# Kernel optimization log

Hardware: AMD Instinct MI355X
Metric: run time of the kernel (lower is better)

Reference implementation:

```python
import jax, jax.numpy as jnp
import numpy as np


def setup_inputs() -> dict:
    key = jax.random.key(0)
    k1, k2, k3 = jax.random.split(key, 3)
    B, C, H, W = 16, 256, 32, 32
    K, D = 8192, 256
    z = jax.random.normal(k1, (B, C, H, W), dtype=jnp.float32)
    # torch init: uniform(-1/K, 1/K); use small-scale values for realism
    embedding = jax.random.uniform(k2, (K, D), dtype=jnp.float32,
                                   minval=-1.0 / K, maxval=1.0 / K)
    proj_w = jax.random.normal(k3, (D, D), dtype=jnp.float32) * (1.0 / np.sqrt(D))
    return {"z": z, "embedding": embedding, "proj_w": proj_w}


def reference(z, embedding, proj_w):
    commitment_cost = 0.25
    B, C, H, W = z.shape
    # codebook = Linear(embedding) with no bias: emb @ W^T  -> [K, D]
    codebook = embedding @ proj_w.T
    zt = jnp.transpose(z, (0, 2, 3, 1))            # [B, H, W, C]
    zf = zt.reshape(-1, C)                          # [N, C], N = B*H*W
    # squared distances: ||z||^2 + ||e||^2 - 2 z.e  -> [N, K]
    d = (jnp.sum(zf * zf, axis=1, keepdims=True)
         + jnp.sum(codebook * codebook, axis=1)
         - 2.0 * jnp.einsum('nd,kd->nk', zf, codebook))
    min_encoding_indices = jnp.argmin(d, axis=1)    # [N]
    z_quantized = codebook[min_encoding_indices].reshape(zt.shape)  # [B,H,W,C]
    commitment_loss = commitment_cost * jnp.mean(
        (jax.lax.stop_gradient(z_quantized) - zt) ** 2)
    codebook_loss = jnp.mean((z_quantized - jax.lax.stop_gradient(zt)) ** 2)
    loss = commitment_loss + codebook_loss
    # straight-through estimator
    zq_st = zt + jax.lax.stop_gradient(z_quantized - zt)
    out = jnp.transpose(zq_st, (0, 3, 1, 2))        # [B, C, H, W]
    idx = min_encoding_indices.reshape(B, H, W)
    return out, loss, commitment_loss, codebook_loss, idx
```

## Files before the change

kernel.cpp:

```cpp
#include <hip/hip_runtime.h>
#include <cfloat>


constexpr int Dd = 256;
constexpr float INV_M = 1.0f / 4194304.0f;
constexpr float DLT = 1e-3f;

typedef unsigned short u16;
typedef unsigned int u32;
typedef __attribute__((ext_vector_type(8))) short short8;
typedef __attribute__((ext_vector_type(4))) float f32x4;

#define GLOBAL_AS __attribute__((address_space(1)))
#define LDS_AS    __attribute__((address_space(3)))

__device__ __forceinline__ unsigned monof(float f) {
  unsigned u = __float_as_uint(f);
  return (u & 0x80000000u) ? ~u : (u | 0x80000000u);
}
__device__ __forceinline__ float unmonof(unsigned p) {
  unsigned u = (p & 0x80000000u) ? (p & 0x7FFFFFFFu) : ~p;
  return __uint_as_float(u);
}
__device__ __forceinline__ u16 f2bf(float x) {
  unsigned u = __float_as_uint(x);
  u += 0x7FFFu + ((u >> 16) & 1u);
  return (u16)(u >> 16);
}

__global__ __launch_bounds__(256)
void k_codebook(const float* __restrict__ emb, const float* __restrict__ proj,
                float* __restrict__ cb, u16* __restrict__ eh) {
  __shared__ float et[64 * 65];
  __shared__ float pt[64 * 65];
  const int t = threadIdx.x;
  const int tx = t & 15, ty = t >> 4;
  const int kb = blockIdx.x * 64;
  const int db = blockIdx.y * 64;
  float acc[4][4];
#pragma unroll
  for (int u = 0; u < 4; ++u)
#pragma unroll
    for (int v = 0; v < 4; ++v) acc[u][v] = 0.f;

  const int jm = t & 15;
  const int q  = t >> 4;

  for (int jc = 0; jc < Dd; jc += 64) {
    __syncthreads();
#pragma unroll
    for (int i = 0; i < 4; ++i) {
      const int row = q + i * 16;
      const float4 e4 = *(const float4*)(emb  + (size_t)(kb + row) * Dd + jc + jm * 4);
      const float4 p4 = *(const float4*)(proj + (size_t)(db + row) * Dd + jc + jm * 4);
      et[(jm*4 + 0) * 65 + row] = e4.x;
      et[(jm*4 + 1) * 65 + row] = e4.y;
      et[(jm*4 + 2) * 65 + row] = e4.z;
      et[(jm*4 + 3) * 65 + row] = e4.w;
      pt[(jm*4 + 0) * 65 + row] = p4.x;
      pt[(jm*4 + 1) * 65 + row] = p4.y;
      pt[(jm*4 + 2) * 65 + row] = p4.z;
      pt[(jm*4 + 3) * 65 + row] = p4.w;
    }
    __syncthreads();
#pragma unroll 16
    for (int j = 0; j < 64; ++j) {
      float a[4], b[4];
#pragma unroll
      for (int u = 0; u < 4; ++u) a[u] = et[j*65 + ty*4 + u];
#pragma unroll
      for (int v = 0; v < 4; ++v) b[v] = pt[j*65 + tx*4 + v];
#pragma unroll
      for (int u = 0; u < 4; ++u)
#pragma unroll
        for (int v = 0; v < 4; ++v) acc[u][v] = fmaf(a[u], b[v], acc[u][v]);
    }
  }
#pragma unroll
  for (int u = 0; u < 4; ++u) {
    const int k = kb + ty*4 + u;
#pragma unroll
    for (int v = 0; v < 4; ++v) {
      const int d = db + tx*4 + v;
      const float val = acc[u][v];
      cb[(size_t)k * Dd + d] = val;
      eh[(size_t)k * Dd + d] = f2bf(val);
    }
  }
}

__global__ __launch_bounds__(256)
void k_norms(const float* __restrict__ cb, float* __restrict__ norms) {
  const int k = blockIdx.x * 256 + threadIdx.x;
  const float* row = cb + (size_t)k * Dd;
  float s = 0.f;
  for (int d = 0; d < Dd; d += 4) {
    const float4 v = *(const float4*)(row + d);
    s = fmaf(v.x, v.x, s);
    s = fmaf(v.y, v.y, s);
    s = fmaf(v.z, v.z, s);
    s = fmaf(v.w, v.w, s);
  }
  norms[k] = s;
}

__global__ __launch_bounds__(256)
void k_prep_z(const float* __restrict__ z, u16* __restrict__ zh,
              float* __restrict__ znorm) {
  __shared__ float tile[256 * 33];
  const int t = threadIdx.x;
  const int blk = blockIdx.x;
  const int w = t & 31, rg = t >> 5;
  const size_t zbase = (size_t)(blk >> 5) * 262144 + (size_t)(blk & 31) * 32 + w;
#pragma unroll 8
  for (int i = 0; i < 32; ++i) {
    const int d = rg * 32 + i;
    tile[d * 33 + w] = z[zbase + (size_t)d * 1024];
  }
  __syncthreads();
  if (t < 32) {
    float s = 0.f;
    for (int d = 0; d < Dd; ++d) {
      const float v = tile[d * 33 + t];
      s = fmaf(v, v, s);
    }
    znorm[blk * 32 + t] = s;
  }
  const int nl = t >> 3, seg = t & 7;
  const size_t obase = (size_t)(blk * 32 + nl) * Dd + seg * 32;
#pragma unroll
  for (int j = 0; j < 4; ++j) {
    u16 hb[8];
#pragma unroll
    for (int e = 0; e < 8; ++e)
      hb[e] = f2bf(tile[(seg * 32 + j * 8 + e) * 33 + nl]);
    *(uint4*)(zh + obase + j * 8) = *(const uint4*)hb;
  }
}

template <bool EMIT>
__global__ __launch_bounds__(256, 2)
void k_scan(const u16* __restrict__ zh, const u16* __restrict__ eh,
            const float* __restrict__ norms, const float* __restrict__ znorm,
            u32* __restrict__ rowminG, const float* __restrict__ rowThr,
            u32* __restrict__ rowcnt, u16* __restrict__ slots) {
  __shared__ u16 zs[64 * 256];
  __shared__ u16 es[256 * 64];
  const int t    = threadIdx.x;
  const int lane = t & 63;
  const int ml   = lane & 15;
  const int qd   = lane >> 4;
  const int wvu  = __builtin_amdgcn_readfirstlane(t >> 6);
  const int rowhalf = wvu & 1;
  const int colhalf = wvu >> 1;
  const int bid  = blockIdx.x;
  const int kb   = (bid & 7) * 1024;
  const int nb   = (bid >> 3) * 64;

#pragma unroll
  for (int i = 0; i < 8; ++i) {
    const int r0 = wvu * 16 + i * 2;
    const int row_l = r0 + (lane >> 5);
    const int c = (lane & 31) ^ ((row_l & 7) << 2);
    const u16* gp = zh + (size_t)(nb + row_l) * 256 + c * 8;
    __builtin_amdgcn_global_load_lds((const GLOBAL_AS void*)gp,
                                     (LDS_AS void*)(zs + r0 * 256), 16, 0, 0);
  }

  float zn[2][4], thr[2][4];
#pragma unroll
  for (int rt = 0; rt < 2; ++rt) {
    const int nr = nb + rowhalf * 32 + rt * 16 + qd * 4;
    const f32x4 z4 = *(const f32x4*)(znorm + nr);
#pragma unroll
    for (int r = 0; r < 4; ++r) zn[rt][r] = z4[r];
    if (EMIT) {
      const f32x4 t4 = *(const f32x4*)(rowThr + nr);
#pragma unroll
      for (int r = 0; r < 4; ++r) thr[rt][r] = t4[r];
    }
  }

  float mv[2][4];
#pragma unroll
  for (int rt = 0; rt < 2; ++rt)
#pragma unroll
    for (int r = 0; r < 4; ++r) mv[rt][r] = FLT_MAX;

#pragma unroll 1
  for (int kt = 0; kt < 4; ++kt) {
    f32x4 acc[2][8];
#pragma unroll
    for (int rt = 0; rt < 2; ++rt)
#pragma unroll
      for (int ct = 0; ct < 8; ++ct) acc[rt][ct] = (f32x4)0.f;

#pragma unroll 1
    for (int dh = 0; dh < 4; ++dh) {
      __syncthreads();
#pragma unroll
      for (int i = 0; i < 8; ++i) {
        const int colbase = wvu * 64 + i * 8;
        const int col_l = colbase + (lane >> 3);
        const int c = (lane & 7) ^ (col_l & 7);
        const u16* gp = eh + (size_t)(kb + kt * 256 + col_l) * 256 + dh * 64 + c * 8;
        __builtin_amdgcn_global_load_lds((const GLOBAL_AS void*)gp,
                                         (LDS_AS void*)(es + colbase * 64), 16, 0, 0);
      }
      __syncthreads();

#pragma unroll
      for (int dc2 = 0; dc2 < 2; ++dc2) {
        short8 Af[2], Bf[8];
#pragma unroll
        for (int rt = 0; rt < 2; ++rt) {
          const int row_l = rowhalf * 32 + rt * 16 + ml;
          const int cg = dh * 8 + dc2 * 4 + qd;
          const int slot = cg ^ ((row_l & 7) << 2);
          Af[rt] = *(const short8*)(zs + row_l * 256 + slot * 8);
        }
#pragma unroll
        for (int ct = 0; ct < 8; ++ct) {
          const int col_l = colhalf * 128 + ct * 16 + ml;
          const int c = dc2 * 4 + qd;
          const int slot = c ^ (col_l & 7);
          Bf[ct] = *(const short8*)(es + col_l * 64 + slot * 8);
        }
#pragma unroll
        for (int rt = 0; rt < 2; ++rt)
#pragma unroll
          for (int ct = 0; ct < 8; ++ct)
            acc[rt][ct] = __builtin_amdgcn_mfma_f32_16x16x32_bf16(
                Af[rt], Bf[ct], acc[rt][ct], 0, 0, 0);
      }
    }

#pragma unroll
    for (int ct = 0; ct < 8; ++ct) {
      const int k = kb + kt * 256 + colhalf * 128 + ct * 16 + ml;
      const float nk = norms[k];
#pragma unroll
      for (int rt = 0; rt < 2; ++rt)
#pragma unroll
        for (int r = 0; r < 4; ++r) {
          const float sc = (zn[rt][r] + nk) - 2.0f * acc[rt][ct][r];
          if (!EMIT) {
            mv[rt][r] = fminf(mv[rt][r], sc);
          } else if (sc <= thr[rt][r]) {
            const int n = nb + rowhalf * 32 + rt * 16 + qd * 4 + r;
            const u32 pos = atomicAdd(&rowcnt[n], 1u);
            if (pos < 32u) slots[n * 32 + pos] = (u16)k;
          }
        }
    }
  }

  if (!EMIT) {
#pragma unroll
    for (int rt = 0; rt < 2; ++rt)
#pragma unroll
      for (int r = 0; r < 4; ++r) {
        float m = mv[rt][r];
#pragma unroll
        for (int s = 1; s < 16; s <<= 1) m = fminf(m, __shfl_xor(m, s, 64));
        if (ml == 0)
          atomicMin(&rowminG[nb + rowhalf * 32 + rt * 16 + qd * 4 + r], monof(m));
      }
  }
}

__global__ __launch_bounds__(256)
void k_thresh(const u32* __restrict__ rowminG, float* __restrict__ rowThr) {
  const int n = blockIdx.x * 256 + threadIdx.x;
  rowThr[n] = unmonof(rowminG[n]) + DLT;
}

__global__ __launch_bounds__(256)
void k_rescore(const float* __restrict__ z, const float* __restrict__ cb,
               const float* __restrict__ norms, const float* __restrict__ znorm,
               const u32* __restrict__ rowcnt, const u16* __restrict__ slots,
               unsigned long long* __restrict__ packed) {
  __shared__ float ztl[32 * 261];
  const int t = threadIdx.x;
  const int blk = blockIdx.x;
  const int w = t & 31, dg = t >> 5;
  const size_t zbase = (size_t)(blk >> 5) * 262144 + (size_t)(blk & 31) * 32;
#pragma unroll 8
  for (int i = 0; i < 32; ++i) {
    const int d = dg * 32 + i;
    ztl[w * 261 + d] = z[zbase + (size_t)d * 1024 + w];
  }
  __syncthreads();

  const int lane = t & 63;
  const int wv = t >> 6;
#pragma unroll 1
  for (int i = 0; i < 8; ++i) {
    const int rl = wv * 8 + i;
    const int n = blk * 32 + rl;
    const u32 cnt = min(rowcnt[n], 32u);
    const float znr = znorm[n];
    unsigned long long best = 0xFFFFFFFFFFFFFFFFull;
    for (u32 c = 0; c < cnt; ++c) {
      const int k = (int)slots[n * 32 + c];
      const float4 c4 = *(const float4*)(cb + (size_t)k * Dd + lane * 4);
      const float* zp = ztl + rl * 261 + lane * 4;
      float p = 0.f;
      p = fmaf(zp[0], c4.x, p);
      p = fmaf(zp[1], c4.y, p);
      p = fmaf(zp[2], c4.z, p);
      p = fmaf(zp[3], c4.w, p);
#pragma unroll
      for (int s = 1; s < 64; s <<= 1) p += __shfl_xor(p, s, 64);
      const float sc = (znr + norms[k]) - 2.0f * p;
      const unsigned long long pk =
          ((unsigned long long)monof(sc) << 32) | (unsigned)k;
      if (pk < best) best = pk;
    }
    if (lane == 0 && cnt > 0) packed[n] = best;
  }
}

__global__ __launch_bounds__(256)
void k_output(const float* __restrict__ z, const float* __restrict__ cb,
              const unsigned long long* __restrict__ packed,
              float* __restrict__ out, float* __restrict__ idxf,
              float* __restrict__ ssum) {
  __shared__ float zqT[256 * 33];
  __shared__ float part[4];
  const int t = threadIdx.x;
  const int blk = blockIdx.x;
  const int nbase = blk * 32;

  {
    const int nl = t >> 3, m = t & 7;
    const int idx = (int)(packed[nbase + nl] & 0xFFFFFFFFull);
    const float* row = cb + (size_t)idx * Dd;
#pragma unroll
    for (int i = 0; i < 8; ++i) {
      const int d0 = m * 4 + i * 32;
      const float4 v = *(const float4*)(row + d0);
      zqT[(d0 + 0) * 33 + nl] = v.x;
      zqT[(d0 + 1) * 33 + nl] = v.y;
      zqT[(d0 + 2) * 33 + nl] = v.z;
      zqT[(d0 + 3) * 33 + nl] = v.w;
    }
    if (t < 32)
      idxf[nbase + t] = (float)(unsigned)(packed[nbase + t] & 0xFFFFFFFFull);
  }
  __syncthreads();

  const int w = t & 31, cg = t >> 5;
  const size_t base = (size_t)(blk >> 5) * 262144 + (size_t)(blk & 31) * 32 + w;
  float local = 0.f;
#pragma unroll
  for (int cc = 0; cc < 32; ++cc) {
    const int c = cg * 32 + cc;
    const float q  = zqT[c * 33 + w];
    const float zv = z[base + (size_t)c * 1024];
    out[base + (size_t)c * 1024] = q;
    const float dd = q - zv;
    local = fmaf(dd, dd, local);
  }
  float v = local;
#pragma unroll
  for (int m = 1; m < 64; m <<= 1) v += __shfl_xor(v, m, 64);
  if ((t & 63) == 0) part[t >> 6] = v;
  __syncthreads();
  if (t == 0) atomicAdd(ssum, part[0] + part[1] + part[2] + part[3]);
}

__global__ void k_final(const float* __restrict__ ssum, float* __restrict__ scal) {
  const float m = *ssum * INV_M;
  scal[0] = 1.25f * m;
  scal[1] = 0.25f * m;
  scal[2] = m;
}

extern "C" void kernel_launch(void* const* d_in, const int* in_sizes, int n_in,
                              void* d_out, int out_size, void* d_ws, size_t ws_size,
                              hipStream_t stream) {
  const float* z    = (const float*)d_in[0];
  const float* emb  = (const float*)d_in[1];
  const float* proj = (const float*)d_in[2];

  float* out  = (float*)d_out;
  float* scal = out + 4194304;
  float* idxf = out + 4194307;

  float* cb    = (float*)d_ws;
  float* norms = cb + 2097152;
  unsigned long long* packed =
      (unsigned long long*)(norms + 8192);
  float* znorm = (float*)(packed + 16384);
  u16* zh = (u16*)(znorm + 16384);
  u16* eh = zh + 4194304;
  u32* rowminG = (u32*)(eh + 2097152);
  float* rowThr = (float*)(rowminG + 16384);
  u32* rowcnt = (u32*)(rowThr + 16384);
  u16* slots = (u16*)(rowcnt + 16384);
  float* ssum = (float*)(slots + 16384 * 32);

  hipMemsetAsync(rowminG, 0xFF, 16384 * sizeof(u32), stream);
  hipMemsetAsync(rowcnt, 0, 16384 * sizeof(u32), stream);
  hipMemsetAsync(packed, 0xFF, 16384 * sizeof(unsigned long long), stream);
  hipMemsetAsync(ssum, 0, sizeof(float), stream);

  k_codebook<<<dim3(128, 4), 256, 0, stream>>>(emb, proj, cb, eh);
  k_norms   <<<32, 256, 0, stream>>>(cb, norms);
  k_prep_z  <<<512, 256, 0, stream>>>(z, zh, znorm);
  k_scan<false><<<2048, 256, 0, stream>>>(zh, eh, norms, znorm,
                                          rowminG, rowThr, rowcnt, slots);
  k_thresh  <<<64, 256, 0, stream>>>(rowminG, rowThr);
  k_scan<true> <<<2048, 256, 0, stream>>>(zh, eh, norms, znorm,
                                          rowminG, rowThr, rowcnt, slots);
  k_rescore <<<512, 256, 0, stream>>>(z, cb, norms, znorm, rowcnt, slots, packed);
  k_output  <<<512, 256, 0, stream>>>(z, cb, packed, out, idxf, ssum);
  k_final   <<<1, 1, 0, stream>>>(ssum, scal);

  (void)in_sizes; (void)n_in; (void)out_size; (void)ws_size;
}
```

Before: 400.2 us.

## Keep z fragments in registers and double-buffer codebook tiles in scan kernel

Restructures k_scan so each wave loads its full set of z bf16 A-fragments (64 rows x 256 dims) into registers once, instead of staging them through LDS. Codebook tiles are staged in 32-wide depth chunks into a double-buffered LDS array, so the next chunk's global-to-LDS load overlaps with the current chunk's MFMAs, and there is one barrier per step instead of two. The per-row z norm is dropped from the score because it does not change the per-row argmin or the threshold comparison. This trades a large register footprint (A fragments plus accumulators) against LDS traffic and sync stalls, which may pressure occupancy.

```diff
diff --git a/kernel.cpp b/kernel.cpp
--- a/kernel.cpp
+++ b/kernel.cpp
@@ -138,116 +138,105 @@
   }
 }
 
+__device__ __forceinline__ void stage_es(const u16* __restrict__ eh, u16* esb,
+                                         int KB, int d0, int wv, int lane) {
+#pragma unroll
+  for (int i = 0; i < 4; ++i) {
+    const int cb0 = (wv * 4 + i) * 16;
+    const int col_l = cb0 + (lane >> 2);
+    const int cgl = ((lane & 3) - ((col_l >> 1) & 3)) & 3;
+    const u16* gp = eh + (size_t)(KB + col_l) * 256 + d0 + cgl * 8;
+    __builtin_amdgcn_global_load_lds((const GLOBAL_AS void*)gp,
+                                     (LDS_AS void*)(esb + cb0 * 32), 16, 0, 0);
+  }
+}
+
 template <bool EMIT>
 __global__ __launch_bounds__(256, 2)
 void k_scan(const u16* __restrict__ zh, const u16* __restrict__ eh,
-            const float* __restrict__ norms, const float* __restrict__ znorm,
+            const float* __restrict__ norms,
             u32* __restrict__ rowminG, const float* __restrict__ rowThr,
             u32* __restrict__ rowcnt, u16* __restrict__ slots) {
-  __shared__ u16 zs[64 * 256];
-  __shared__ u16 es[256 * 64];
+  __shared__ u16 es[2][8192];
   const int t    = threadIdx.x;
   const int lane = t & 63;
   const int ml   = lane & 15;
   const int qd   = lane >> 4;
-  const int wvu  = __builtin_amdgcn_readfirstlane(t >> 6);
-  const int rowhalf = wvu & 1;
-  const int colhalf = wvu >> 1;
+  const int wv   = __builtin_amdgcn_readfirstlane(t >> 6);
   const int bid  = blockIdx.x;
   const int kb   = (bid & 7) * 1024;
   const int nb   = (bid >> 3) * 64;
 
-#pragma unroll
-  for (int i = 0; i < 8; ++i) {
-    const int r0 = wvu * 16 + i * 2;
-    const int row_l = r0 + (lane >> 5);
-    const int c = (lane & 31) ^ ((row_l & 7) << 2);
-    const u16* gp = zh + (size_t)(nb + row_l) * 256 + c * 8;
-    __builtin_amdgcn_global_load_lds((const GLOBAL_AS void*)gp,
-                                     (LDS_AS void*)(zs + r0 * 256), 16, 0, 0);
-  }
-
-  float zn[2][4], thr[2][4];
-#pragma unroll
-  for (int rt = 0; rt < 2; ++rt) {
-    const int nr = nb + rowhalf * 32 + rt * 16 + qd * 4;
-    const f32x4 z4 = *(const f32x4*)(znorm + nr);
-#pragma unroll
-    for (int r = 0; r < 4; ++r) zn[rt][r] = z4[r];
+  short8 A[4][8];
+#pragma unroll
+  for (int rt = 0; rt < 4; ++rt)
+#pragma unroll
+    for (int dh = 0; dh < 8; ++dh)
+      A[rt][dh] = *(const short8*)(zh + (size_t)(nb + rt * 16 + ml) * 256
+                                      + dh * 32 + qd * 8);
+
+  float thr[4][4];
+  float mv[4][4];
+#pragma unroll
+  for (int rt = 0; rt < 4; ++rt) {
     if (EMIT) {
-      const f32x4 t4 = *(const f32x4*)(rowThr + nr);
+      const f32x4 t4 = *(const f32x4*)(rowThr + nb + rt * 16 + qd * 4);
 #pragma unroll
       for (int r = 0; r < 4; ++r) thr[rt][r] = t4[r];
-    }
-  }
-
-  float mv[2][4];
-#pragma unroll
-  for (int rt = 0; rt < 2; ++rt)
-#pragma unroll
-    for (int r = 0; r < 4; ++r) mv[rt][r] = FLT_MAX;
+    } else {
+#pragma unroll
+      for (int r = 0; r < 4; ++r) mv[rt][r] = FLT_MAX;
+    }
+  }
+
+  stage_es(eh, es[0], kb, 0, wv, lane);
+  __syncthreads();
 
 #pragma unroll 1
   for (int kt = 0; kt < 4; ++kt) {
-    f32x4 acc[2][8];
-#pragma unroll
-    for (int rt = 0; rt < 2; ++rt)
-#pragma unroll
-      for (int ct = 0; ct < 8; ++ct) acc[rt][ct] = (f32x4)0.f;
-
-#pragma unroll 1
-    for (int dh = 0; dh < 4; ++dh) {
+    f32x4 acc[4][4];
+#pragma unroll
+    for (int rt = 0; rt < 4; ++rt)
+#pragma unroll
+      for (int ct = 0; ct < 4; ++ct) acc[rt][ct] = (f32x4)0.f;
+
+#pragma unroll
+    for (int dh = 0; dh < 8; ++dh) {
+      const int p = kt * 8 + dh;
+      if (p < 31)
+        stage_es(eh, es[(p + 1) & 1], kb + ((p + 1) >> 3) * 256,
+                 ((p + 1) & 7) * 32, wv, lane);
+      const u16* esb = es[p & 1];
+      short8 B[4];
+#pragma unroll
+      for (int ct = 0; ct < 4; ++ct) {
+        const int col_l = wv * 64 + ct * 16 + ml;
+        const int slot = (qd + ((col_l >> 1) & 3)) & 3;
+        B[ct] = *(const short8*)(esb + col_l * 32 + slot * 8);
+      }
+#pragma unroll
+      for (int ct = 0; ct < 4; ++ct)
+#pragma unroll
+        for (int rt = 0; rt < 4; ++rt)
+          acc[rt][ct] = __builtin_amdgcn_mfma_f32_16x16x32_bf16(
+              A[rt][dh], B[ct], acc[rt][ct], 0, 0, 0);
       __syncthreads();
-#pragma unroll
-      for (int i = 0; i < 8; ++i) {
-        const int colbase = wvu * 64 + i * 8;
-        const int col_l = colbase + (lane >> 3);
-        const int c = (lane & 7) ^ (col_l & 7);
-        const u16* gp = eh + (size_t)(kb + kt * 256 + col_l) * 256 + dh * 64 + c * 8;
-        __builtin_amdgcn_global_load_lds((const GLOBAL_AS void*)gp,
-                                         (LDS_AS void*)(es + colbase * 64), 16, 0, 0);
-      }
-      __syncthreads();
-
-#pragma unroll
-      for (int dc2 = 0; dc2 < 2; ++dc2) {
-        short8 Af[2], Bf[8];
-#pragma unroll
-        for (int rt = 0; rt < 2; ++rt) {
-          const int row_l = rowhalf * 32 + rt * 16 + ml;
-          const int cg = dh * 8 + dc2 * 4 + qd;
-          const int slot = cg ^ ((row_l & 7) << 2);
-          Af[rt] = *(const short8*)(zs + row_l * 256 + slot * 8);
-        }
-#pragma unroll
-        for (int ct = 0; ct < 8; ++ct) {
-          const int col_l = colhalf * 128 + ct * 16 + ml;
-          const int c = dc2 * 4 + qd;
-          const int slot = c ^ (col_l & 7);
-          Bf[ct] = *(const short8*)(es + col_l * 64 + slot * 8);
-        }
-#pragma unroll
-        for (int rt = 0; rt < 2; ++rt)
-#pragma unroll
-          for (int ct = 0; ct < 8; ++ct)
-            acc[rt][ct] = __builtin_amdgcn_mfma_f32_16x16x32_bf16(
-                Af[rt], Bf[ct], acc[rt][ct], 0, 0, 0);
-      }
-    }
-
-#pragma unroll
-    for (int ct = 0; ct < 8; ++ct) {
-      const int k = kb + kt * 256 + colhalf * 128 + ct * 16 + ml;
+    }
+
+    const int KB = kb + kt * 256;
+#pragma unroll
+    for (int ct = 0; ct < 4; ++ct) {
+      const int k = KB + wv * 64 + ct * 16 + ml;
       const float nk = norms[k];
 #pragma unroll
-      for (int rt = 0; rt < 2; ++rt)
+      for (int rt = 0; rt < 4; ++rt)
 #pragma unroll
         for (int r = 0; r < 4; ++r) {
-          const float sc = (zn[rt][r] + nk) - 2.0f * acc[rt][ct][r];
+          const float sc = fmaf(-2.0f, acc[rt][ct][r], nk);
           if (!EMIT) {
             mv[rt][r] = fminf(mv[rt][r], sc);
           } else if (sc <= thr[rt][r]) {
-            const int n = nb + rowhalf * 32 + rt * 16 + qd * 4 + r;
+            const int n = nb + rt * 16 + qd * 4 + r;
             const u32 pos = atomicAdd(&rowcnt[n], 1u);
             if (pos < 32u) slots[n * 32 + pos] = (u16)k;
           }
@@ -257,14 +246,14 @@
 
   if (!EMIT) {
 #pragma unroll
-    for (int rt = 0; rt < 2; ++rt)
+    for (int rt = 0; rt < 4; ++rt)
 #pragma unroll
       for (int r = 0; r < 4; ++r) {
         float m = mv[rt][r];
 #pragma unroll
         for (int s = 1; s < 16; s <<= 1) m = fminf(m, __shfl_xor(m, s, 64));
         if (ml == 0)
-          atomicMin(&rowminG[nb + rowhalf * 32 + rt * 16 + qd * 4 + r], monof(m));
+          atomicMin(&rowminG[nb + rt * 16 + qd * 4 + r], monof(m));
       }
   }
 }
@@ -409,10 +398,10 @@
   k_codebook<<<dim3(128, 4), 256, 0, stream>>>(emb, proj, cb, eh);
   k_norms   <<<32, 256, 0, stream>>>(cb, norms);
   k_prep_z  <<<512, 256, 0, stream>>>(z, zh, znorm);
-  k_scan<false><<<2048, 256, 0, stream>>>(zh, eh, norms, znorm,
+  k_scan<false><<<2048, 256, 0, stream>>>(zh, eh, norms,
                                           rowminG, rowThr, rowcnt, slots);
   k_thresh  <<<64, 256, 0, stream>>>(rowminG, rowThr);
-  k_scan<true> <<<2048, 256, 0, stream>>>(zh, eh, norms, znorm,
+  k_scan<true> <<<2048, 256, 0, stream>>>(zh, eh, norms,
                                           rowminG, rowThr, rowcnt, slots);
   k_rescore <<<512, 256, 0, stream>>>(z, cb, norms, znorm, rowcnt, slots, packed);
   k_output  <<<512, 256, 0, stream>>>(z, cb, packed, out, idxf, ssum);
```

After: 429.6 us. 7.3% more time.
